# Kernel optimization log

Measured on AMD Instinct MI355X. Metric: run time of the kernel, lower is better.

The kernel has to match this reference:

```python
import jax, jax.numpy as jnp
import numpy as np
import math

B, H, S, D = 8, 16, 1024, 64


def setup_inputs() -> dict:
    key = jax.random.key(0)
    kq, kk, kv, kl = jax.random.split(key, 4)
    queries = jax.random.normal(kq, (B * H, S, D), dtype=jnp.float32)
    keys = jax.random.normal(kk, (B * H, S, D), dtype=jnp.float32)
    values = jax.random.normal(kv, (B * H, S, D), dtype=jnp.float32)
    valid_lens = jax.random.randint(kl, (B,), 0, 1024, dtype=jnp.int64)
    return {"queries": queries, "keys": keys, "values": values, "valid_lens": valid_lens}


def reference(queries, keys, values, valid_lens):
    d = queries.shape[-1]
    seq_len = queries.shape[1]
    b = valid_lens.shape[0]
    h = queries.shape[0] // b
    scale = 1.0 / math.sqrt(d)
    # [BH, S, S] scores, faithful to bmm(q, k^T)/sqrt(d)
    scores = jnp.einsum("bqd,bkd->bqk", queries, keys) * scale
    # encode_mask: mask[b, q, k] = (k >= valid_lens[b]) for 1-D valid_lens
    key_mask = jnp.arange(seq_len) >= valid_lens[:, None]  # [B, S]
    scores = scores.reshape(b, h, seq_len, seq_len)
    # masked_fill with 1e-6 (NOT -inf), faithful to the original
    scores = jnp.where(key_mask[:, None, None, :], jnp.float32(1e-6), scores)
    attn = jax.nn.softmax(scores, axis=-1)
    out = jnp.einsum("bhqk,bhkd->bhqd", attn, values.reshape(b, h, seq_len, d))
    return out.reshape(b * h, seq_len, d)
```

## Files before the change

kernel.cpp:

```cpp
#include <hip/hip_runtime.h>
#include <hip/hip_bf16.h>

typedef short short4v __attribute__((ext_vector_type(4)));
typedef short short8v __attribute__((ext_vector_type(8)));
typedef float floatx4 __attribute__((ext_vector_type(4)));
typedef unsigned int uint2v __attribute__((ext_vector_type(2)));

#define SLEN 1024
#define DDIM 64
#define NBH  128

__device__ __forceinline__ unsigned short f2bf(float f) {
  union { float f; unsigned int u; } v; v.f = f;
  unsigned int u = v.u;
  u += 0x7fffu + ((u >> 16) & 1u);
  return (unsigned short)(u >> 16);
}

__device__ __forceinline__ unsigned int pkbf(float a, float b) {
  __hip_bfloat162 h = __float22bfloat162_rn(float2{a, b});
  union { __hip_bfloat162 h; unsigned int u; } c; c.h = h;
  return c.u;
}

__device__ __forceinline__ void pl32sw(unsigned int &a, unsigned int &b) {
#if __has_builtin(__builtin_amdgcn_permlane32_swap)
  uint2v r = __builtin_amdgcn_permlane32_swap(a, b, false, false);
  a = r[0]; b = r[1];
#else
  asm volatile("s_nop 1\n\tv_permlane32_swap_b32 %0, %1" : "+v"(a), "+v"(b));
#endif
}
__device__ __forceinline__ void pl16sw(unsigned int &a, unsigned int &b) {
#if __has_builtin(__builtin_amdgcn_permlane16_swap)
  uint2v r = __builtin_amdgcn_permlane16_swap(a, b, false, false);
  a = r[0]; b = r[1];
#else
  asm volatile("s_nop 1\n\tv_permlane16_swap_b32 %0, %1" : "+v"(a), "+v"(b));
#endif
}

__device__ __forceinline__ int decode_vl(const int* __restrict__ vraw, int bh) {
  const bool is64 = (vraw[1] == 0) && (vraw[3] == 0) && (vraw[5] == 0) && (vraw[7] == 0);
  const int b = bh >> 4;
  return is64 ? vraw[2 * b] : vraw[b];
}

__global__ __launch_bounds__(64)
void prep_cs(const float* __restrict__ Vg, float* __restrict__ CS,
             const int* __restrict__ vraw) {
  const int tile = blockIdx.x;
  const int bh = tile >> 4, ch = tile & 15;
  const int d = threadIdx.x;
  const int vl = decode_vl(vraw, bh);
  const int ts = (vl >> 6) + ((vl & 63) ? 1 : 0);
  float sum = 0.f;
  if (ch >= ts) {
    const float* src = Vg + (size_t)(bh * SLEN + ch * 64) * DDIM + d;
    float s0 = 0.f, s1 = 0.f, s2 = 0.f, s3 = 0.f;
    #pragma unroll
    for (int k = 0; k < 64; k += 4) {
      s0 += src[(size_t)(k + 0) * DDIM];
      s1 += src[(size_t)(k + 1) * DDIM];
      s2 += src[(size_t)(k + 2) * DDIM];
      s3 += src[(size_t)(k + 3) * DDIM];
    }
    sum = (s0 + s1) + (s2 + s3);
  }
  CS[(size_t)tile * 64 + d] = sum;
}

__global__ __launch_bounds__(64)
void prep_sv(float* __restrict__ CS, const int* __restrict__ vraw, int* __restrict__ SRT) {
  const int blk = blockIdx.x;
  if (blk < NBH) {
    const int d = threadIdx.x;
    float acc = 0.f;
    for (int ch = 15; ch >= 0; --ch) {
      const size_t idx = ((size_t)blk * 16 + ch) * 64 + d;
      acc += CS[idx];
      CS[idx] = acc;
    }
  } else {
    const int x = threadIdx.x;
    if (x < 8) {
      int key[16];
      #pragma unroll
      for (int k = 0; k < 16; ++k) {
        const int vv = decode_vl(vraw, x + 8 * k);
        key[k] = (vv >> 6) + ((vv & 63) ? 1 : 0);
      }
      #pragma unroll
      for (int i = 0; i < 16; ++i) {
        int rank = 0;
        #pragma unroll
        for (int k2 = 0; k2 < 16; ++k2)
          rank += (int)((key[k2] > key[i]) || (key[k2] == key[i] && k2 < i));
        SRT[x * 16 + rank] = x + 8 * i;
      }
    }
  }
}

__global__ __launch_bounds__(256)
void attn_main(const float* __restrict__ Qg, const float* __restrict__ Kg,
               const float* __restrict__ Vg, const float* __restrict__ SV,
               const int* __restrict__ SRT, const int* __restrict__ vraw,
               float* __restrict__ Og)
{
  __shared__ unsigned short K_lds[2][4096];
  __shared__ unsigned short VT_lds[2][4096];

  const int t  = threadIdx.x;
  const int ww = t >> 6;
  const int ln = t & 15;
  const int g  = (t >> 4) & 3;

  int bh, q0;
  if (SRT) {
    const int xcd  = blockIdx.x & 7;
    const int lidx = blockIdx.x >> 3;
    const int cu   = lidx & 31;
    const int j    = lidx >> 5;
    const int r    = j * 32 + ((j & 1) ? (31 - cu) : cu);
    bh = SRT[xcd * 16 + (r >> 3)];
    q0 = (r & 7) * 128;
  } else {
    bh = blockIdx.x & 127;
    q0 = (blockIdx.x >> 7) * 128;
  }

  const int vl          = decode_vl(vraw, bh);
  const int full_ch     = vl >> 6;
  const int has_partial = (vl & 63) ? 1 : 0;
  const int nch         = SV ? (full_ch + has_partial) : 16;
  const int tail_start  = full_ch + has_partial;

  const float qs = 0.125f * 1.44269504f;
  short8v bq[2][2];
  #pragma unroll
  for (int nt = 0; nt < 2; ++nt) {
    const float* qp = Qg + ((size_t)bh * SLEN + q0 + ww * 32 + nt * 16 + ln) * DDIM;
    #pragma unroll
    for (int st = 0; st < 2; ++st) {
      const float4 f0 = *(const float4*)(qp + st * 32 + g * 8);
      const float4 f1 = *(const float4*)(qp + st * 32 + g * 8 + 4);
      short8v a;
      a[0]=(short)f2bf(f0.x*qs); a[1]=(short)f2bf(f0.y*qs);
      a[2]=(short)f2bf(f0.z*qs); a[3]=(short)f2bf(f0.w*qs);
      a[4]=(short)f2bf(f1.x*qs); a[5]=(short)f2bf(f1.y*qs);
      a[6]=(short)f2bf(f1.z*qs); a[7]=(short)f2bf(f1.w*qs);
      bq[nt][st] = a;
    }
  }

  const int l7  = ln & 7;
  const int sw0 = ((g) ^ l7) * 8;
  const int sw1 = ((4 + g) ^ l7) * 8;

  short8v ones;
  #pragma unroll
  for (int j = 0; j < 8; ++j) ones[j] = (short)0x3F80;

  floatx4 ot[2][4], lacc[2];
  #pragma unroll
  for (int m = 0; m < 2; ++m) {
    lacc[m] = (floatx4){0.f, 0.f, 0.f, 0.f};
    #pragma unroll
    for (int f = 0; f < 4; ++f) ot[m][f] = (floatx4){0.f, 0.f, 0.f, 0.f};
  }

  float kr[2][8];
  float vlo[8], vhi[8];
  const int dv = t & 31;
  const int gv = t >> 5;

  const float* kbB = Kg + (size_t)bh * SLEN * DDIM;
  const float* vbB = Vg + (size_t)bh * SLEN * DDIM;

  auto stage_load = [&](int ch) {
    const float* kb_ = kbB + (size_t)ch * 64 * DDIM;
    const float* vb_ = vbB + (size_t)ch * 64 * DDIM;
    #pragma unroll
    for (int h = 0; h < 2; ++h) {
      const int q = t + h * 256;
      const int r = q >> 3, gr = q & 7;
      const float4 f0 = *(const float4*)(kb_ + r * DDIM + gr * 8);
      const float4 f1 = *(const float4*)(kb_ + r * DDIM + gr * 8 + 4);
      kr[h][0]=f0.x; kr[h][1]=f0.y; kr[h][2]=f0.z; kr[h][3]=f0.w;
      kr[h][4]=f1.x; kr[h][5]=f1.y; kr[h][6]=f1.z; kr[h][7]=f1.w;
    }
    #pragma unroll
    for (int j = 0; j < 8; ++j) {
      vlo[j] = vb_[(gv * 8 + j) * DDIM + dv];
      vhi[j] = vb_[(gv * 8 + j) * DDIM + dv + 32];
    }
  };
  auto stage_write = [&](int b) {
    #pragma unroll
    for (int h = 0; h < 2; ++h) {
      const int q = t + h * 256;
      const int r = q >> 3, gr = q & 7;
      union { short8v s; unsigned int u[4]; } ks;
      ks.u[0] = pkbf(kr[h][0], kr[h][1]);
      ks.u[1] = pkbf(kr[h][2], kr[h][3]);
      ks.u[2] = pkbf(kr[h][4], kr[h][5]);
      ks.u[3] = pkbf(kr[h][6], kr[h][7]);
      *(short8v*)&K_lds[b][r * 64 + ((gr ^ (r & 7)) * 8)] = ks.s;
    }
    union { short8v s; unsigned int u[4]; } va, vb2;
    va.u[0]  = pkbf(vlo[0], vlo[1]); va.u[1]  = pkbf(vlo[2], vlo[3]);
    va.u[2]  = pkbf(vlo[4], vlo[5]); va.u[3]  = pkbf(vlo[6], vlo[7]);
    vb2.u[0] = pkbf(vhi[0], vhi[1]); vb2.u[1] = pkbf(vhi[2], vhi[3]);
    vb2.u[2] = pkbf(vhi[4], vhi[5]); vb2.u[3] = pkbf(vhi[6], vhi[7]);
    const int swv = (gv ^ (dv & 7)) * 8;
    *(short8v*)&VT_lds[b][dv * 64 + swv] = va.s;
    *(short8v*)&VT_lds[b][(dv + 32) * 64 + swv] = vb2.s;
  };

  if (nch > 0) {
    stage_load(0);
    stage_write(0);
    if (nch > 1) stage_load(1);
    asm volatile("s_waitcnt lgkmcnt(0)" ::: "memory");
    __builtin_amdgcn_s_barrier();
    asm volatile("" ::: "memory");
  }

  for (int ch = 0; ch < nch; ++ch) {
    const int b = ch & 1;
    if (ch + 1 < nch) stage_write(b ^ 1);
    if (ch + 2 < nch) stage_load(ch + 2);

    floatx4 c[4][2];
    __builtin_amdgcn_s_setprio(1);
    #pragma unroll
    for (int mt = 0; mt < 4; ++mt) {
      const short8v a0 = *(const short8v*)&K_lds[b][(mt * 16 + ln) * 64 + sw0];
      const short8v a1 = *(const short8v*)&K_lds[b][(mt * 16 + ln) * 64 + sw1];
      #pragma unroll
      for (int nt = 0; nt < 2; ++nt) {
        floatx4 acc = (floatx4){0.f, 0.f, 0.f, 0.f};
        acc = __builtin_amdgcn_mfma_f32_16x16x32_bf16(a0, bq[nt][0], acc, 0, 0, 0);
        acc = __builtin_amdgcn_mfma_f32_16x16x32_bf16(a1, bq[nt][1], acc, 0, 0, 0);
        c[mt][nt] = acc;
      }
    }
    __builtin_amdgcn_s_setprio(0);

    unsigned int pk0[4][2], pk1[4][2];
    const bool fullv = (ch < full_ch);
    #pragma unroll
    for (int mt = 0; mt < 4; ++mt) {
      const int kg = ch * 64 + mt * 16 + g * 4;
      #pragma unroll
      for (int nt = 0; nt < 2; ++nt) {
        float p[4];
        if (fullv) {
          #pragma unroll
          for (int i = 0; i < 4; ++i) p[i] = __builtin_amdgcn_exp2f(c[mt][nt][i]);
        } else {
          #pragma unroll
          for (int i = 0; i < 4; ++i) {
            const float x = (kg + i < vl) ? c[mt][nt][i] : 0.0f;
            p[i] = __builtin_amdgcn_exp2f(x);
          }
        }
        pk0[mt][nt] = pkbf(p[0], p[1]);
        pk1[mt][nt] = pkbf(p[2], p[3]);
      }
    }

    short8v bp[2][2];
    #pragma unroll
    for (int st = 0; st < 2; ++st) {
      #pragma unroll
      for (int nt = 0; nt < 2; ++nt) {
        unsigned int a0 = pk0[2 * st][nt], b0 = pk0[2 * st + 1][nt];
        unsigned int a1 = pk1[2 * st][nt], b1 = pk1[2 * st + 1][nt];
        pl32sw(a0, b0); pl16sw(a0, b0);
        pl32sw(a1, b1); pl16sw(a1, b1);
        union { short8v s; unsigned int u[4]; } bb;
        bb.u[0] = a0; bb.u[1] = a1; bb.u[2] = b0; bb.u[3] = b1;
        bp[st][nt] = bb.s;
      }
    }

    __builtin_amdgcn_s_setprio(1);
    #pragma unroll
    for (int st = 0; st < 2; ++st) {
      lacc[0] = __builtin_amdgcn_mfma_f32_16x16x32_bf16(ones, bp[st][0], lacc[0], 0, 0, 0);
      lacc[1] = __builtin_amdgcn_mfma_f32_16x16x32_bf16(ones, bp[st][1], lacc[1], 0, 0, 0);
      const int sw = (st == 0) ? sw0 : sw1;
      #pragma unroll
      for (int f = 0; f < 4; ++f) {
        const short8v av = *(const short8v*)&VT_lds[b][(f * 16 + ln) * 64 + sw];
        ot[0][f] = __builtin_amdgcn_mfma_f32_16x16x32_bf16(av, bp[st][0], ot[0][f], 0, 0, 0);
        ot[1][f] = __builtin_amdgcn_mfma_f32_16x16x32_bf16(av, bp[st][1], ot[1][f], 0, 0, 0);
      }
    }
    __builtin_amdgcn_s_setprio(0);

    if (ch + 1 < nch) {
      asm volatile("s_waitcnt lgkmcnt(0)" ::: "memory");
      __builtin_amdgcn_s_barrier();
      asm volatile("" ::: "memory");
    }
  }

  if (SV != nullptr && tail_start < 16) {
    const float* sv = SV + ((size_t)bh * 16 + tail_start) * 64 + g * 4;
    float4 sv4[4];
    #pragma unroll
    for (int f = 0; f < 4; ++f) sv4[f] = *(const float4*)(sv + f * 16);
    const float ml = (float)(SLEN - tail_start * 64);
    #pragma unroll
    for (int nt = 0; nt < 2; ++nt) {
      #pragma unroll
      for (int i = 0; i < 4; ++i) lacc[nt][i] += ml;
      #pragma unroll
      for (int f = 0; f < 4; ++f) {
        ot[nt][f][0] += sv4[f].x; ot[nt][f][1] += sv4[f].y;
        ot[nt][f][2] += sv4[f].z; ot[nt][f][3] += sv4[f].w;
      }
    }
  }

  #pragma unroll
  for (int nt = 0; nt < 2; ++nt) {
    const float inv = 1.0f / lacc[nt][0];
    float* orow = Og + ((size_t)bh * SLEN + q0 + ww * 32 + nt * 16 + ln) * DDIM + g * 4;
    #pragma unroll
    for (int f = 0; f < 4; ++f) {
      float4 v4;
      v4.x = ot[nt][f][0] * inv; v4.y = ot[nt][f][1] * inv;
      v4.z = ot[nt][f][2] * inv; v4.w = ot[nt][f][3] * inv;
      *(float4*)(orow + f * 16) = v4;
    }
  }
}

extern "C" void kernel_launch(void* const* d_in, const int* in_sizes, int n_in,
                              void* d_out, int out_size, void* d_ws, size_t ws_size,
                              hipStream_t stream) {
  const float* Q = (const float*)d_in[0];
  const float* K = (const float*)d_in[1];
  const float* V = (const float*)d_in[2];
  const int*  vl = (const int*)d_in[3];
  float* out = (float*)d_out;

  const size_t ws_cs  = (size_t)NBH * 16 * 64 * 4;
  const size_t ws_all = ws_cs + 8 * 16 * 4;

  if (ws_size >= ws_all) {
    float* CS = (float*)d_ws;
    int*  SRT = (int*)((char*)d_ws + ws_cs);
    prep_cs<<<2048, 64, 0, stream>>>(V, CS, vl);
    prep_sv<<<NBH + 1, 64, 0, stream>>>(CS, vl, SRT);
    attn_main<<<dim3(1024), dim3(256), 0, stream>>>(Q, K, V, CS, SRT, vl, out);
  } else {
    attn_main<<<dim3(1024), dim3(256), 0, stream>>>(Q, K, V, nullptr, nullptr, vl, out);
  }
}
```

Measured before the change: 160.5 us.

## Double query tile per block to 256 rows with 512-thread workgroups

Each attention workgroup now handles 256 query rows with 8 waves instead of 128 rows with 4 waves. The grid is halved and the sorted-head block mapping is adjusted to match. Each K/V chunk is loaded from global memory, converted to bf16 and staged in LDS once for twice as many queries, with each thread staging a single K row segment and one V column. This is meant to cut redundant global K/V traffic and conversion work, at the cost of fewer, larger blocks. That risks coarser load balance across CUs given the uneven valid lengths, and adds barrier cost across 8 waves.

```diff
diff --git a/kernel.cpp b/kernel.cpp
--- a/kernel.cpp
+++ b/kernel.cpp
@@ -45,6 +45,10 @@
   const int b = bh >> 4;
   return is64 ? vraw[2 * b] : vraw[b];
 }
+__device__ __forceinline__ int nch_of(const int* __restrict__ vraw, int bh) {
+  const int v = decode_vl(vraw, bh);
+  return (v >> 6) + ((v & 63) ? 1 : 0);
+}
 
 __global__ __launch_bounds__(64)
 void prep_cs(const float* __restrict__ Vg, float* __restrict__ CS,
@@ -52,8 +56,7 @@
   const int tile = blockIdx.x;
   const int bh = tile >> 4, ch = tile & 15;
   const int d = threadIdx.x;
-  const int vl = decode_vl(vraw, bh);
-  const int ts = (vl >> 6) + ((vl & 63) ? 1 : 0);
+  const int ts = nch_of(vraw, bh);
   float sum = 0.f;
   if (ch >= ts) {
     const float* src = Vg + (size_t)(bh * SLEN + ch * 64) * DDIM + d;
@@ -86,10 +89,7 @@
     if (x < 8) {
       int key[16];
       #pragma unroll
-      for (int k = 0; k < 16; ++k) {
-        const int vv = decode_vl(vraw, x + 8 * k);
-        key[k] = (vv >> 6) + ((vv & 63) ? 1 : 0);
-      }
+      for (int k = 0; k < 16; ++k) key[k] = nch_of(vraw, x + 8 * k);
       #pragma unroll
       for (int i = 0; i < 16; ++i) {
         int rank = 0;
@@ -102,7 +102,7 @@
   }
 }
 
-__global__ __launch_bounds__(256)
+__global__ __launch_bounds__(512)
 void attn_main(const float* __restrict__ Qg, const float* __restrict__ Kg,
                const float* __restrict__ Vg, const float* __restrict__ SV,
                const int* __restrict__ SRT, const int* __restrict__ vraw,
@@ -123,11 +123,11 @@
     const int cu   = lidx & 31;
     const int j    = lidx >> 5;
     const int r    = j * 32 + ((j & 1) ? (31 - cu) : cu);
-    bh = SRT[xcd * 16 + (r >> 3)];
-    q0 = (r & 7) * 128;
+    bh = SRT[xcd * 16 + (r >> 2)];
+    q0 = (r & 3) * 256;
   } else {
     bh = blockIdx.x & 127;
-    q0 = (blockIdx.x >> 7) * 128;
+    q0 = (blockIdx.x >> 7) * 256;
   }
 
   const int vl          = decode_vl(vraw, bh);
@@ -170,52 +170,34 @@
     for (int f = 0; f < 4; ++f) ot[m][f] = (floatx4){0.f, 0.f, 0.f, 0.f};
   }
 
-  float kr[2][8];
-  float vlo[8], vhi[8];
-  const int dv = t & 31;
-  const int gv = t >> 5;
-
+  float kr[8];
+  float vcol[8];
+  const int kra_r = t >> 3, kra_g = t & 7;
+  const int dv = t & 63;
+  const int gv = t >> 6;
   const float* kbB = Kg + (size_t)bh * SLEN * DDIM;
   const float* vbB = Vg + (size_t)bh * SLEN * DDIM;
 
   auto stage_load = [&](int ch) {
     const float* kb_ = kbB + (size_t)ch * 64 * DDIM;
     const float* vb_ = vbB + (size_t)ch * 64 * DDIM;
-    #pragma unroll
-    for (int h = 0; h < 2; ++h) {
-      const int q = t + h * 256;
-      const int r = q >> 3, gr = q & 7;
-      const float4 f0 = *(const float4*)(kb_ + r * DDIM + gr * 8);
-      const float4 f1 = *(const float4*)(kb_ + r * DDIM + gr * 8 + 4);
-      kr[h][0]=f0.x; kr[h][1]=f0.y; kr[h][2]=f0.z; kr[h][3]=f0.w;
-      kr[h][4]=f1.x; kr[h][5]=f1.y; kr[h][6]=f1.z; kr[h][7]=f1.w;
-    }
-    #pragma unroll
-    for (int j = 0; j < 8; ++j) {
-      vlo[j] = vb_[(gv * 8 + j) * DDIM + dv];
-      vhi[j] = vb_[(gv * 8 + j) * DDIM + dv + 32];
-    }
+    const float4 f0 = *(const float4*)(kb_ + kra_r * DDIM + kra_g * 8);
+    const float4 f1 = *(const float4*)(kb_ + kra_r * DDIM + kra_g * 8 + 4);
+    kr[0]=f0.x; kr[1]=f0.y; kr[2]=f0.z; kr[3]=f0.w;
+    kr[4]=f1.x; kr[5]=f1.y; kr[6]=f1.z; kr[7]=f1.w;
+    #pragma unroll
+    for (int j = 0; j < 8; ++j)
+      vcol[j] = vb_[(gv * 8 + j) * DDIM + dv];
   };
   auto stage_write = [&](int b) {
-    #pragma unroll
-    for (int h = 0; h < 2; ++h) {
-      const int q = t + h * 256;
-      const int r = q >> 3, gr = q & 7;
-      union { short8v s; unsigned int u[4]; } ks;
-      ks.u[0] = pkbf(kr[h][0], kr[h][1]);
-      ks.u[1] = pkbf(kr[h][2], kr[h][3]);
-      ks.u[2] = pkbf(kr[h][4], kr[h][5]);
-      ks.u[3] = pkbf(kr[h][6], kr[h][7]);
-      *(short8v*)&K_lds[b][r * 64 + ((gr ^ (r & 7)) * 8)] = ks.s;
-    }
-    union { short8v s; unsigned int u[4]; } va, vb2;
-    va.u[0]  = pkbf(vlo[0], vlo[1]); va.u[1]  = pkbf(vlo[2], vlo[3]);
-    va.u[2]  = pkbf(vlo[4], vlo[5]); va.u[3]  = pkbf(vlo[6], vlo[7]);
-    vb2.u[0] = pkbf(vhi[0], vhi[1]); vb2.u[1] = pkbf(vhi[2], vhi[3]);
-    vb2.u[2] = pkbf(vhi[4], vhi[5]); vb2.u[3] = pkbf(vhi[6], vhi[7]);
-    const int swv = (gv ^ (dv & 7)) * 8;
-    *(short8v*)&VT_lds[b][dv * 64 + swv] = va.s;
-    *(short8v*)&VT_lds[b][(dv + 32) * 64 + swv] = vb2.s;
+    union { short8v s; unsigned int u[4]; } ks;
+    ks.u[0] = pkbf(kr[0], kr[1]); ks.u[1] = pkbf(kr[2], kr[3]);
+    ks.u[2] = pkbf(kr[4], kr[5]); ks.u[3] = pkbf(kr[6], kr[7]);
+    *(short8v*)&K_lds[b][kra_r * 64 + ((kra_g ^ (kra_r & 7)) * 8)] = ks.s;
+    union { short8v s; unsigned int u[4]; } vs;
+    vs.u[0] = pkbf(vcol[0], vcol[1]); vs.u[1] = pkbf(vcol[2], vcol[3]);
+    vs.u[2] = pkbf(vcol[4], vcol[5]); vs.u[3] = pkbf(vcol[6], vcol[7]);
+    *(short8v*)&VT_lds[b][dv * 64 + ((gv ^ (dv & 7)) * 8)] = vs.s;
   };
 
   if (nch > 0) {
@@ -353,12 +335,12 @@
   const size_t ws_all = ws_cs + 8 * 16 * 4;
 
   if (ws_size >= ws_all) {
-    float* CS = (float*)d_ws;
-    int*  SRT = (int*)((char*)d_ws + ws_cs);
+    float* CS  = (float*)d_ws;
+    int*   SRT = (int*)((char*)d_ws + ws_cs);
     prep_cs<<<2048, 64, 0, stream>>>(V, CS, vl);
     prep_sv<<<NBH + 1, 64, 0, stream>>>(CS, vl, SRT);
-    attn_main<<<dim3(1024), dim3(256), 0, stream>>>(Q, K, V, CS, SRT, vl, out);
+    attn_main<<<dim3(512), dim3(512), 0, stream>>>(Q, K, V, CS, SRT, vl, out);
   } else {
-    attn_main<<<dim3(1024), dim3(256), 0, stream>>>(Q, K, V, nullptr, nullptr, vl, out);
-  }
-}
+    attn_main<<<dim3(512), dim3(512), 0, stream>>>(Q, K, V, nullptr, nullptr, vl, out);
+  }
+}
```

After: 152.1 us. 1.06x faster.
